# Kernel optimization log

Hardware: AMD Instinct MI355X
Metric: run time of the kernel (lower is better)

The kernel has to match this reference:

```python
import jax, jax.numpy as jnp
import numpy as np

B, S, D, H = 4, 4096, 2048, 16
DH = D // H
SCALE = float(np.sqrt(DH))


def setup_inputs() -> dict:
    key = jax.random.key(0)
    ks = jax.random.split(key, 11)
    std = 1.0 / np.sqrt(D)
    inp = {
        "query": jax.random.normal(ks[0], (B, S, D), jnp.float32),
        "key": jax.random.normal(ks[1], (B, S, D), jnp.float32),
        "value": jax.random.normal(ks[2], (B, S, D), jnp.float32),
        "Wq": jax.random.normal(ks[3], (D, D), jnp.float32) * std,
        "bq": jax.random.normal(ks[4], (D,), jnp.float32) * std,
        "Wk": jax.random.normal(ks[5], (D, D), jnp.float32) * std,
        "bk": jax.random.normal(ks[6], (D,), jnp.float32) * std,
        "Wv": jax.random.normal(ks[7], (D, D), jnp.float32) * std,
        "bv": jax.random.normal(ks[8], (D,), jnp.float32) * std,
        "Wo": jax.random.normal(ks[9], (D, D), jnp.float32) * std,
        "bo": jax.random.normal(ks[10], (D,), jnp.float32) * std,
    }
    return inp


def reference(query, key, value, Wq, bq, Wk, bk, Wv, bv, Wo, bo):
    # Linear projections (torch nn.Linear: x @ W^T + b)
    Q = query @ Wq.T + bq          # [B,S,D]
    K = key @ Wk.T + bk
    V = value @ Wv.T + bv
    Q = Q.reshape(B, S, H, DH)
    K = K.reshape(B, S, H, DH)
    V = V.reshape(B, S, H, DH)
    # NOTE: original torch code does NOT transpose heads to dim 1, so the
    # matmul contracts over head-dim pairs at each position: scores [B,S,H,H]
    scores = jnp.einsum('bsid,bsjd->bsij', Q, K) / SCALE
    attention = jax.nn.softmax(scores, axis=-1)   # softmax over heads (faithful)
    x = jnp.einsum('bsij,bsjd->bsid', attention, V)  # [B,S,H,DH]
    # permute(0,2,1,3) -> [B,H,S,DH], then view(B,-1,D) -> [B,S,D]
    x = jnp.transpose(x, (0, 2, 1, 3)).reshape(B, S, D)
    out = x @ Wo.T + bo
    return out, attention
```

## Files before the change

kernel.cpp:

```cpp
#include <hip/hip_runtime.h>


#define DEV __device__ __forceinline__

using short8  = __attribute__((ext_vector_type(8))) short;
using ushort8 = __attribute__((ext_vector_type(8))) unsigned short;
using f32x4   = __attribute__((ext_vector_type(4))) float;

constexpr int BATCH = 4, SEQ = 4096, DIM = 2048, NH = 16, DHD = 128;
constexpr int GM = BATCH * SEQ;
constexpr int GN = DIM, GK = DIM;

DEV unsigned short f2bf(float f) {
  unsigned int u = __builtin_bit_cast(unsigned int, f);
  u += 0x7FFFu + ((u >> 16) & 1u);
  return (unsigned short)(u >> 16);
}
DEV float bf2f(unsigned short h) {
  unsigned int u = ((unsigned int)h) << 16;
  return __builtin_bit_cast(float, u);
}

DEV void gload16(const void* g, void* l) {
  __builtin_amdgcn_global_load_lds(
      (const __attribute__((address_space(1))) void*)g,
      (__attribute__((address_space(3))) void*)l, 16, 0, 0);
}

__global__ void cvt_f32_bf16(const float* __restrict__ src,
                             unsigned short* __restrict__ dst, int n) {
  int i = (blockIdx.x * blockDim.x + threadIdx.x) * 4;
  if (i >= n) return;
  f32x4 f = *(const f32x4*)(src + i);
  ushort4 o;
  o.x = f2bf(f[0]); o.y = f2bf(f[1]); o.z = f2bf(f[2]); o.w = f2bf(f[3]);
  *(ushort4*)(dst + i) = o;
}

template <bool AF32, bool OUTF32>
__global__ __launch_bounds__(256)
void gemm_bt(const void* __restrict__ Ap, const unsigned short* __restrict__ Bp,
             const float* __restrict__ bias, void* __restrict__ Cp) {
  constexpr int BM = 128, BN = 128, BK = 32;
  __shared__ unsigned short As[BM * BK];
  __shared__ unsigned short Bs[BN * BK];

  const int tid  = threadIdx.x;
  const int lane = tid & 63;
  const int wv   = tid >> 6;

  constexpr int NWG = (GM / BM) * (GN / BN);
  int bid = (int)blockIdx.x;
  bid = (bid & 7) * (NWG >> 3) + (bid >> 3);
  const int mt = bid >> 4;
  const int nt = bid & 15;
  const int bm0 = mt * BM, bn0 = nt * BN;

  const int wr = wv >> 1, wc = wv & 1;
  const int r16 = lane & 15, kblk = lane >> 4;

  f32x4 acc[4][4] = {};

  const int srow = lane >> 2;
  const int scol = (lane & 3) * 8;

  for (int k0 = 0; k0 < GK; k0 += BK) {
    if (k0) __syncthreads();
#pragma unroll
    for (int c = 0; c < 2; ++c) {
      const int chunk = wv * 2 + c;
      const unsigned short* g =
          Bp + (size_t)(bn0 + chunk * 16 + srow) * GK + (k0 + scol);
      gload16(g, &Bs[chunk * 512]);
    }
    if constexpr (AF32) {
      const float* Af = (const float*)Ap;
      const int arow = tid >> 1;
      const int ak = (tid & 1) * 16;
      const f32x4* g4 = (const f32x4*)(Af + (size_t)(bm0 + arow) * GK + k0 + ak);
      f32x4 f[4];
      f[0] = g4[0]; f[1] = g4[1]; f[2] = g4[2]; f[3] = g4[3];
      ushort8 p0, p1;
#pragma unroll
      for (int j = 0; j < 8; ++j) {
        p0[j] = f2bf(f[j >> 2][j & 3]);
        p1[j] = f2bf(f[2 + (j >> 2)][j & 3]);
      }
      *(ushort8*)&As[arow * BK + ak]     = p0;
      *(ushort8*)&As[arow * BK + ak + 8] = p1;
    } else {
#pragma unroll
      for (int c = 0; c < 2; ++c) {
        const int chunk = wv * 2 + c;
        const unsigned short* g = (const unsigned short*)Ap +
            (size_t)(bm0 + chunk * 16 + srow) * GK + (k0 + scol);
        gload16(g, &As[chunk * 512]);
      }
    }
    __syncthreads();
    short8 af[4], bf[4];
#pragma unroll
    for (int m = 0; m < 4; ++m)
      af[m] = *(const short8*)&As[(wr * 64 + m * 16 + r16) * BK + kblk * 8];
#pragma unroll
    for (int n = 0; n < 4; ++n)
      bf[n] = *(const short8*)&Bs[(wc * 64 + n * 16 + r16) * BK + kblk * 8];
#pragma unroll
    for (int m = 0; m < 4; ++m)
#pragma unroll
      for (int n = 0; n < 4; ++n)
        acc[m][n] = __builtin_amdgcn_mfma_f32_16x16x32_bf16(af[m], bf[n],
                                                            acc[m][n], 0, 0, 0);
  }
  const int rb = (lane >> 4) * 4;
#pragma unroll
  for (int m = 0; m < 4; ++m) {
#pragma unroll
    for (int i = 0; i < 4; ++i) {
      const size_t row = bm0 + wr * 64 + m * 16 + rb + i;
#pragma unroll
      for (int n = 0; n < 4; ++n) {
        const int col = bn0 + wc * 64 + n * 16 + r16;
        float v = acc[m][n][i] + bias[col];
        if constexpr (OUTF32)
          ((float*)Cp)[row * GN + col] = v;
        else
          ((unsigned short*)Cp)[row * GN + col] = f2bf(v);
      }
    }
  }
}

using u16x8 = __attribute__((ext_vector_type(8))) unsigned short;

__global__ __launch_bounds__(256)
void attn_kernel(const unsigned short* __restrict__ Qb,
                 const unsigned short* __restrict__ Kb,
                 const unsigned short* __restrict__ Vb,
                 float* __restrict__ attnOut,
                 unsigned short* __restrict__ X2) {
  __shared__ float qf[16 * 128];
  __shared__ float kf[16 * 132];
  __shared__ float vf[16 * 128];
  __shared__ float sc[256];

  const int t = threadIdx.x;
  const int p = blockIdx.x;
  const size_t rowoff = (size_t)p * DIM;

  {
    const int e = t * 8;
    u16x8 qv = *(const u16x8*)(Qb + rowoff + e);
    u16x8 kv = *(const u16x8*)(Kb + rowoff + e);
    u16x8 vv = *(const u16x8*)(Vb + rowoff + e);
    const int r = t >> 4, c = (t & 15) * 8;
#pragma unroll
    for (int j = 0; j < 8; ++j) qf[r * 128 + c + j] = bf2f(qv[j]);
#pragma unroll
    for (int j = 0; j < 8; ++j) kf[r * 132 + c + j] = bf2f(kv[j]);
#pragma unroll
    for (int j = 0; j < 8; ++j) vf[r * 128 + c + j] = bf2f(vv[j]);
  }
  __syncthreads();

  const int i = t >> 4, j = t & 15;
  float s = 0.f;
#pragma unroll
  for (int d4 = 0; d4 < 32; ++d4) {
    f32x4 q4 = *(const f32x4*)&qf[i * 128 + d4 * 4];
    f32x4 k4 = *(const f32x4*)&kf[j * 132 + d4 * 4];
    s = fmaf(q4[0], k4[0], fmaf(q4[1], k4[1], fmaf(q4[2], k4[2], fmaf(q4[3], k4[3], s))));
  }
  s *= 0.08838834764831845f;

  float mx = s;
#pragma unroll
  for (int off = 8; off; off >>= 1) mx = fmaxf(mx, __shfl_xor(mx, off, 16));
  float ex = __expf(s - mx);
  float sum = ex;
#pragma unroll
  for (int off = 8; off; off >>= 1) sum += __shfl_xor(sum, off, 16);
  float a = ex / sum;

  attnOut[(size_t)p * 256 + t] = a;
  sc[t] = a;
  __syncthreads();

  const int dh0 = j * 8;
  float o[8] = {};
#pragma unroll
  for (int jj = 0; jj < 16; ++jj) {
    float aij = sc[i * 16 + jj];
#pragma unroll
    for (int e2 = 0; e2 < 8; ++e2)
      o[e2] = fmaf(aij, vf[jj * 128 + dh0 + e2], o[e2]);
  }
  const int b = p >> 12, spos = p & 4095;
  const int row = i * 256 + (spos >> 4);
  const int col = ((spos & 15) << 7) + dh0;
  ushort8 pk;
#pragma unroll
  for (int e2 = 0; e2 < 8; ++e2) pk[e2] = f2bf(o[e2]);
  *(ushort8*)(X2 + (size_t)b * (SEQ * DIM) + (size_t)row * DIM + col) = pk;
}

extern "C" void kernel_launch(void* const* d_in, const int* in_sizes, int n_in,
                              void* d_out, int out_size, void* d_ws,
                              size_t ws_size, hipStream_t stream) {
  const float* q  = (const float*)d_in[0];
  const float* k  = (const float*)d_in[1];
  const float* v  = (const float*)d_in[2];
  const float* Wq = (const float*)d_in[3];
  const float* bq = (const float*)d_in[4];
  const float* Wk = (const float*)d_in[5];
  const float* bk = (const float*)d_in[6];
  const float* Wv = (const float*)d_in[7];
  const float* bv = (const float*)d_in[8];
  const float* Wo = (const float*)d_in[9];
  const float* bo = (const float*)d_in[10];

  const size_t NE = (size_t)GM * GK;
  const size_t WE = (size_t)GK * GN;

  unsigned short* ws16 = (unsigned short*)d_ws;
  unsigned short* Wq_b = ws16;
  unsigned short* Wk_b = Wq_b + WE;
  unsigned short* Wv_b = Wk_b + WE;
  unsigned short* Wo_b = Wv_b + WE;
  unsigned short* Qb   = Wo_b + WE;
  unsigned short* Kb   = Qb + NE;
  unsigned short* Vb   = Kb + NE;
  unsigned short* X2   = Vb + NE;
  unsigned short* Qin  = X2 + NE;
  unsigned short* Kin  = Qin + NE;
  unsigned short* Vin  = Kin + NE;

  const size_t need_small = (4 * WE + 4 * NE) * 2;
  const size_t need_big   = need_small + 3 * NE * 2;
  const bool big = ws_size >= need_big;

  float* outMain = (float*)d_out;
  float* attnOut = outMain + (size_t)GM * GN;

  cvt_f32_bf16<<<WE / 1024, 256, 0, stream>>>(Wq, Wq_b, (int)WE);
  cvt_f32_bf16<<<WE / 1024, 256, 0, stream>>>(Wk, Wk_b, (int)WE);
  cvt_f32_bf16<<<WE / 1024, 256, 0, stream>>>(Wv, Wv_b, (int)WE);
  cvt_f32_bf16<<<WE / 1024, 256, 0, stream>>>(Wo, Wo_b, (int)WE);

  constexpr int GEMM_GRID = (GM / 128) * (GN / 128);

  if (big) {
    cvt_f32_bf16<<<NE / 1024, 256, 0, stream>>>(q, Qin, (int)NE);
    cvt_f32_bf16<<<NE / 1024, 256, 0, stream>>>(k, Kin, (int)NE);
    cvt_f32_bf16<<<NE / 1024, 256, 0, stream>>>(v, Vin, (int)NE);
    gemm_bt<false, false><<<GEMM_GRID, 256, 0, stream>>>(Qin, Wq_b, bq, Qb);
    gemm_bt<false, false><<<GEMM_GRID, 256, 0, stream>>>(Kin, Wk_b, bk, Kb);
    gemm_bt<false, false><<<GEMM_GRID, 256, 0, stream>>>(Vin, Wv_b, bv, Vb);
  } else {
    gemm_bt<true, false><<<GEMM_GRID, 256, 0, stream>>>(q, Wq_b, bq, Qb);
    gemm_bt<true, false><<<GEMM_GRID, 256, 0, stream>>>(k, Wk_b, bk, Kb);
    gemm_bt<true, false><<<GEMM_GRID, 256, 0, stream>>>(v, Wv_b, bv, Vb);
  }

  attn_kernel<<<GM, 256, 0, stream>>>(Qb, Kb, Vb, attnOut, X2);

  gemm_bt<false, true><<<GEMM_GRID, 256, 0, stream>>>(X2, Wo_b, bo, outMain);
}
```

Before: 956.2 us.

## Add 256x256 double-buffered swizzled-LDS GEMM with interleaved loads and MFMA phases

Introduces a new 512-thread GEMM with 256x256 tiles, BK=64, double-buffered LDS filled by direct global-to-LDS loads with an XOR swizzle, and four MFMA phases interleaved with prefetch of the next K tile. Priority boosts and explicit waitcnt/barriers schedule the phases. It replaces the 128x128 single-buffered GEMM for the QKV projections (big-workspace path) and the output projection, aiming at higher data reuse and overlap of memory with compute. The larger tiles cut the grid to 512 blocks and raise register pressure, which can limit occupancy and leave some CUs less evenly loaded.

```diff
diff --git a/kernel.cpp b/kernel.cpp
--- a/kernel.cpp
+++ b/kernel.cpp
@@ -6,8 +6,9 @@
 using short8  = __attribute__((ext_vector_type(8))) short;
 using ushort8 = __attribute__((ext_vector_type(8))) unsigned short;
 using f32x4   = __attribute__((ext_vector_type(4))) float;
-
-constexpr int BATCH = 4, SEQ = 4096, DIM = 2048, NH = 16, DHD = 128;
+using u16x8   = __attribute__((ext_vector_type(8))) unsigned short;
+
+constexpr int BATCH = 4, SEQ = 4096, DIM = 2048;
 constexpr int GM = BATCH * SEQ;
 constexpr int GN = DIM, GK = DIM;
 
@@ -26,6 +27,11 @@
       (const __attribute__((address_space(1))) void*)g,
       (__attribute__((address_space(3))) void*)l, 16, 0, 0);
 }
+
+#define BAR    __builtin_amdgcn_s_barrier()
+#define LGKM0  asm volatile("s_waitcnt lgkmcnt(0)" ::: "memory")
+#define VMCNT4 asm volatile("s_waitcnt vmcnt(4)" ::: "memory")
+#define SCHED0 __builtin_amdgcn_sched_barrier(0)
 
 __global__ void cvt_f32_bf16(const float* __restrict__ src,
                              unsigned short* __restrict__ dst, int n) {
@@ -37,6 +43,164 @@
   *(ushort4*)(dst + i) = o;
 }
 
+template <bool OUTF32>
+__global__ __launch_bounds__(512)
+void gemm256(const unsigned short* __restrict__ Ap,
+             const unsigned short* __restrict__ Bp,
+             const float* __restrict__ bias, void* __restrict__ Cp) {
+  constexpr int BK = 64, KT = GK / BK;
+  __shared__ unsigned short As[2][256 * BK];
+  __shared__ unsigned short Bs[2][256 * BK];
+
+  const int tid  = threadIdx.x;
+  const int lane = tid & 63;
+  const int wv   = tid >> 6;
+  const int wm   = wv >> 2, wn = wv & 3;
+
+  int bid = (int)blockIdx.x;
+  int swz = (bid & 7) * 64 + (bid >> 3);
+  const int mt = swz & 63, nt = swz >> 6;
+  const int bm0 = mt * 256, bn0 = nt * 256;
+
+  int dstoff[4];
+  size_t offA[4], offB[4];
+#pragma unroll
+  for (int r = 0; r < 4; ++r) {
+    int d = tid * 16 + r * 8192;
+    int s = d ^ (((d >> 7) & 7) << 4);
+    int row = s >> 7, col = (s & 127) >> 1;
+    dstoff[r] = d;
+    offA[r] = (size_t)(bm0 + row) * GK + col;
+    offB[r] = (size_t)(bn0 + row) * GK + col;
+  }
+
+  const int r16 = lane & 15, kb = (lane >> 4) * 16;
+  const int arow = wm * 128 + r16;
+  const int brow = wn * 64 + r16;
+
+  f32x4 acc[8][4] = {};
+  short8 af[4][2], bl[2][2], bh[2][2];
+
+  auto stA = [&](int buf, int kt, int r) {
+    gload16(Ap + offA[r] + (size_t)kt * BK, (char*)&As[buf][0] + dstoff[r]);
+  };
+  auto stB = [&](int buf, int kt, int r) {
+    gload16(Bp + offB[r] + (size_t)kt * BK, (char*)&Bs[buf][0] + dstoff[r]);
+  };
+  auto ldf = [&](const unsigned short* base, int row, int ks) -> short8 {
+    int a = (row * 128 + ks * 64 + kb) ^ ((row & 7) << 4);
+    return *(const short8*)((const char*)base + a);
+  };
+
+#pragma unroll
+  for (int r = 0; r < 4; ++r) stA(0, 0, r);
+#pragma unroll
+  for (int r = 0; r < 4; ++r) stB(0, 0, r);
+#pragma unroll
+  for (int r = 0; r < 4; ++r) stA(1, 1, r);
+  VMCNT4;
+  BAR;
+
+  for (int kt = 0; kt < KT; ++kt) {
+    const int cb = kt & 1, nb = cb ^ 1;
+    const unsigned short* Ab = &As[cb][0];
+    const unsigned short* Bb = &Bs[cb][0];
+
+#pragma unroll
+    for (int m = 0; m < 4; ++m) {
+      af[m][0] = ldf(Ab, arow + m * 16, 0);
+      af[m][1] = ldf(Ab, arow + m * 16, 1);
+    }
+#pragma unroll
+    for (int n = 0; n < 2; ++n) {
+      bl[n][0] = ldf(Bb, brow + n * 16, 0);
+      bl[n][1] = ldf(Bb, brow + n * 16, 1);
+    }
+    if (kt + 1 < KT) { stB(nb, kt + 1, 0); stB(nb, kt + 1, 1); }
+    BAR; LGKM0; SCHED0;
+    __builtin_amdgcn_s_setprio(1);
+#pragma unroll
+    for (int m = 0; m < 4; ++m)
+#pragma unroll
+      for (int n = 0; n < 2; ++n) {
+        acc[m][n] = __builtin_amdgcn_mfma_f32_16x16x32_bf16(af[m][0], bl[n][0], acc[m][n], 0, 0, 0);
+        acc[m][n] = __builtin_amdgcn_mfma_f32_16x16x32_bf16(af[m][1], bl[n][1], acc[m][n], 0, 0, 0);
+      }
+    __builtin_amdgcn_s_setprio(0);
+    BAR;
+
+#pragma unroll
+    for (int n = 0; n < 2; ++n) {
+      bh[n][0] = ldf(Bb, brow + 32 + n * 16, 0);
+      bh[n][1] = ldf(Bb, brow + 32 + n * 16, 1);
+    }
+    if (kt + 1 < KT) { stB(nb, kt + 1, 2); stB(nb, kt + 1, 3); }
+    BAR; LGKM0; SCHED0;
+    __builtin_amdgcn_s_setprio(1);
+#pragma unroll
+    for (int m = 0; m < 4; ++m)
+#pragma unroll
+      for (int n = 0; n < 2; ++n) {
+        acc[m][2 + n] = __builtin_amdgcn_mfma_f32_16x16x32_bf16(af[m][0], bh[n][0], acc[m][2 + n], 0, 0, 0);
+        acc[m][2 + n] = __builtin_amdgcn_mfma_f32_16x16x32_bf16(af[m][1], bh[n][1], acc[m][2 + n], 0, 0, 0);
+      }
+    __builtin_amdgcn_s_setprio(0);
+    BAR;
+
+#pragma unroll
+    for (int m = 0; m < 4; ++m) {
+      af[m][0] = ldf(Ab, arow + 64 + m * 16, 0);
+      af[m][1] = ldf(Ab, arow + 64 + m * 16, 1);
+    }
+    if (kt + 2 < KT) { stA(cb, kt + 2, 0); stA(cb, kt + 2, 2); }
+    BAR; LGKM0; SCHED0;
+    __builtin_amdgcn_s_setprio(1);
+#pragma unroll
+    for (int m = 0; m < 4; ++m)
+#pragma unroll
+      for (int n = 0; n < 2; ++n) {
+        acc[4 + m][2 + n] = __builtin_amdgcn_mfma_f32_16x16x32_bf16(af[m][0], bh[n][0], acc[4 + m][2 + n], 0, 0, 0);
+        acc[4 + m][2 + n] = __builtin_amdgcn_mfma_f32_16x16x32_bf16(af[m][1], bh[n][1], acc[4 + m][2 + n], 0, 0, 0);
+      }
+    __builtin_amdgcn_s_setprio(0);
+    BAR;
+
+    if (kt + 2 < KT) { stA(cb, kt + 2, 1); stA(cb, kt + 2, 3); }
+    VMCNT4;
+    BAR;
+    __builtin_amdgcn_s_setprio(1);
+#pragma unroll
+    for (int m = 0; m < 4; ++m)
+#pragma unroll
+      for (int n = 0; n < 2; ++n) {
+        acc[4 + m][n] = __builtin_amdgcn_mfma_f32_16x16x32_bf16(af[m][0], bl[n][0], acc[4 + m][n], 0, 0, 0);
+        acc[4 + m][n] = __builtin_amdgcn_mfma_f32_16x16x32_bf16(af[m][1], bl[n][1], acc[4 + m][n], 0, 0, 0);
+      }
+    __builtin_amdgcn_s_setprio(0);
+    BAR;
+  }
+
+  float bs[4];
+#pragma unroll
+  for (int n = 0; n < 4; ++n) bs[n] = bias[bn0 + wn * 64 + n * 16 + r16];
+  const int rb = (lane >> 4) * 4;
+#pragma unroll
+  for (int m = 0; m < 8; ++m)
+#pragma unroll
+    for (int i = 0; i < 4; ++i) {
+      const size_t row = (size_t)bm0 + wm * 128 + m * 16 + rb + i;
+#pragma unroll
+      for (int n = 0; n < 4; ++n) {
+        const int col = bn0 + wn * 64 + n * 16 + r16;
+        float v = acc[m][n][i] + bs[n];
+        if constexpr (OUTF32)
+          ((float*)Cp)[row * GN + col] = v;
+        else
+          ((unsigned short*)Cp)[row * GN + col] = f2bf(v);
+      }
+    }
+}
+
 template <bool AF32, bool OUTF32>
 __global__ __launch_bounds__(256)
 void gemm_bt(const void* __restrict__ Ap, const unsigned short* __restrict__ Bp,
@@ -98,23 +262,23 @@
       }
     }
     __syncthreads();
-    short8 af[4], bf[4];
-#pragma unroll
-    for (int m = 0; m < 4; ++m)
-      af[m] = *(const short8*)&As[(wr * 64 + m * 16 + r16) * BK + kblk * 8];
+    short8 a_f[4], b_f[4];
+#pragma unroll
+    for (int m = 0; m < 4; ++m)
+      a_f[m] = *(const short8*)&As[(wr * 64 + m * 16 + r16) * BK + kblk * 8];
 #pragma unroll
     for (int n = 0; n < 4; ++n)
-      bf[n] = *(const short8*)&Bs[(wc * 64 + n * 16 + r16) * BK + kblk * 8];
+      b_f[n] = *(const short8*)&Bs[(wc * 64 + n * 16 + r16) * BK + kblk * 8];
 #pragma unroll
     for (int m = 0; m < 4; ++m)
 #pragma unroll
       for (int n = 0; n < 4; ++n)
-        acc[m][n] = __builtin_amdgcn_mfma_f32_16x16x32_bf16(af[m], bf[n],
+        acc[m][n] = __builtin_amdgcn_mfma_f32_16x16x32_bf16(a_f[m], b_f[n],
                                                             acc[m][n], 0, 0, 0);
   }
   const int rb = (lane >> 4) * 4;
 #pragma unroll
-  for (int m = 0; m < 4; ++m) {
+  for (int m = 0; m < 4; ++m)
 #pragma unroll
     for (int i = 0; i < 4; ++i) {
       const size_t row = bm0 + wr * 64 + m * 16 + rb + i;
@@ -128,10 +292,7 @@
           ((unsigned short*)Cp)[row * GN + col] = f2bf(v);
       }
     }
-  }
-}
-
-using u16x8 = __attribute__((ext_vector_type(8))) unsigned short;
+}
 
 __global__ __launch_bounds__(256)
 void attn_kernel(const unsigned short* __restrict__ Qb,
@@ -247,22 +408,23 @@
   cvt_f32_bf16<<<WE / 1024, 256, 0, stream>>>(Wv, Wv_b, (int)WE);
   cvt_f32_bf16<<<WE / 1024, 256, 0, stream>>>(Wo, Wo_b, (int)WE);
 
-  constexpr int GEMM_GRID = (GM / 128) * (GN / 128);
+  constexpr int G256 = (GM / 256) * (GN / 256);
+  constexpr int G128 = (GM / 128) * (GN / 128);
 
   if (big) {
     cvt_f32_bf16<<<NE / 1024, 256, 0, stream>>>(q, Qin, (int)NE);
     cvt_f32_bf16<<<NE / 1024, 256, 0, stream>>>(k, Kin, (int)NE);
     cvt_f32_bf16<<<NE / 1024, 256, 0, stream>>>(v, Vin, (int)NE);
-    gemm_bt<false, false><<<GEMM_GRID, 256, 0, stream>>>(Qin, Wq_b, bq, Qb);
-    gemm_bt<false, false><<<GEMM_GRID, 256, 0, stream>>>(Kin, Wk_b, bk, Kb);
-    gemm_bt<false, false><<<GEMM_GRID, 256, 0, stream>>>(Vin, Wv_b, bv, Vb);
+    gemm256<false><<<G256, 512, 0, stream>>>(Qin, Wq_b, bq, Qb);
+    gemm256<false><<<G256, 512, 0, stream>>>(Kin, Wk_b, bk, Kb);
+    gemm256<false><<<G256, 512, 0, stream>>>(Vin, Wv_b, bv, Vb);
   } else {
-    gemm_bt<true, false><<<GEMM_GRID, 256, 0, stream>>>(q, Wq_b, bq, Qb);
-    gemm_bt<true, false><<<GEMM_GRID, 256, 0, stream>>>(k, Wk_b, bk, Kb);
-    gemm_bt<true, false><<<GEMM_GRID, 256, 0, stream>>>(v, Wv_b, bv, Vb);
+    gemm_bt<true, false><<<G128, 256, 0, stream>>>(q, Wq_b, bq, Qb);
+    gemm_bt<true, false><<<G128, 256, 0, stream>>>(k, Wk_b, bk, Kb);
+    gemm_bt<true, false><<<G128, 256, 0, stream>>>(v, Wv_b, bv, Vb);
   }
 
   attn_kernel<<<GM, 256, 0, stream>>>(Qb, Kb, Vb, attnOut, X2);
 
-  gemm_bt<false, true><<<GEMM_GRID, 256, 0, stream>>>(X2, Wo_b, bo, outMain);
-}
+  gemm256<true><<<G256, 512, 0, stream>>>(X2, Wo_b, bo, outMain);
+}
```

Result: faster. 827.9 us (-13.4%).
